# Kernel tuning notes

Hardware: AMD Instinct MI355X
Metric: run time of the kernel (lower is better)

## Reference

```python
import jax, jax.numpy as jnp
import numpy as np

B, CIN, COUT, H, W, K = 16, 16, 16, 256, 256, 3


def setup_inputs() -> dict:
    key = jax.random.key(0)
    k1, k2, k3 = jax.random.split(key, 3)
    x = jax.random.normal(k1, (B, CIN, H, W), dtype=jnp.float32)
    # complex weights stored as two real tensors (out, in, k, k)
    w_real = jax.random.normal(k2, (COUT, CIN, K, K), dtype=jnp.float32)
    w_imag = jax.random.normal(k3, (COUT, CIN, K, K), dtype=jnp.float32)
    return {"x": x, "w_real": w_real, "w_imag": w_imag}


def reference(x, w_real, w_imag):
    # x: (B, Cin, H, W) real; weights: (Cout, Cin, K, K) complex (as two reals)
    Cout, Cin, k, _ = w_real.shape
    h, w = x.shape[-2], x.shape[-1]
    wc = (w_real + 1j * w_imag).astype(jnp.complex64)
    # zero-pad kernel to (Cout, Cin, H, W); batch dim in the original is redundant
    kp = jnp.zeros((Cout, Cin, h, w), dtype=jnp.complex64).at[:, :, :k, :k].set(wc)
    kernel_freq = jnp.fft.fft2(kp)  # (Cout, Cin, H, W) complex
    # out_freq = x.unsqueeze(1) * kernel_freq; sum over in_channels -> (B, Cout, H, W)
    out = jnp.einsum('bihw,oihw->bohw', x.astype(jnp.complex64), kernel_freq)
    # return complex result as stacked (real, imag): shape (2, B, Cout, H, W)
    return jnp.stack([out.real, out.imag])
```

## Files before the change

### kernel.cpp

```cpp
#include <hip/hip_runtime.h>


constexpr int Hd   = 256;
constexpr int Wd   = 256;
constexpr int Bn   = 16;
constexpr int CIN  = 16;
constexpr int COUT = 16;
constexpr int TW   = 32;
constexpr int NTHREADS = 512;

__global__ __launch_bounds__(NTHREADS)
void freq_conv_kernel(const float* __restrict__ x,
                      const float* __restrict__ wr_g,
                      const float* __restrict__ wi_g,
                      float* __restrict__ out)
{
    __shared__ float xs[Bn * CIN * TW];

    const int tid = threadIdx.x;
    const int bid = blockIdx.x;
    const int h  = bid >> 3;
    const int w0 = (bid & 7) * TW;

    float4 stage[4];
#pragma unroll
    for (int t = 0; t < 4; ++t) {
        int lin = t * NTHREADS + tid;
        int row = lin >> 3;
        int seg = lin & 7;
        stage[t] = *reinterpret_cast<const float4*>(
            &x[(size_t)(row * Hd + h) * Wd + w0 + seg * 4]);
    }

    const int o = tid >> 5;
    const int p = tid & 31;
    const int w = w0 + p;

    const float TWO_PI_OVER_N = 6.28318530717958647692f / 256.0f;
    float sh1, ch1, sw1, cw1;
    __sincosf(TWO_PI_OVER_N * (float)h, &sh1, &ch1);
    __sincosf(TWO_PI_OVER_N * (float)w, &sw1, &cw1);
    const float ch[3] = {1.f, ch1, ch1 * ch1 - sh1 * sh1};
    const float sh[3] = {0.f, sh1, 2.f * sh1 * ch1};
    const float cw[3] = {1.f, cw1, cw1 * cw1 - sw1 * sw1};
    const float sw[3] = {0.f, sw1, 2.f * sw1 * cw1};

    float cph[9], sph[9];
#pragma unroll
    for (int pp = 0; pp < 3; ++pp)
#pragma unroll
        for (int qq = 0; qq < 3; ++qq) {
            cph[pp * 3 + qq] = ch[pp] * cw[qq] - sh[pp] * sw[qq];
            sph[pp * 3 + qq] = sh[pp] * cw[qq] + ch[pp] * sw[qq];
        }

    float Kr[CIN], Ki[CIN];
#pragma unroll
    for (int i = 0; i < CIN; ++i) {
        float kr = 0.f, ki = 0.f;
        const float* wr = &wr_g[(o * CIN + i) * 9];
        const float* wi = &wi_g[(o * CIN + i) * 9];
#pragma unroll
        for (int t = 0; t < 9; ++t) {
            const float a = wr[t], bb = wi[t];
            kr += a * cph[t] + bb * sph[t];
            ki += bb * cph[t] - a * sph[t];
        }
        Kr[i] = kr; Ki[i] = ki;
    }

#pragma unroll
    for (int t = 0; t < 4; ++t) {
        int lin = t * NTHREADS + tid;
        reinterpret_cast<float4*>(xs)[lin] = stage[t];
    }
    __syncthreads();

    const size_t hw = (size_t)h * Wd + w;
#pragma unroll
    for (int b = 0; b < Bn; ++b) {
        float ar = 0.f, ai = 0.f;
#pragma unroll
        for (int i = 0; i < CIN; ++i) {
            const float xv = xs[(b * CIN + i) * TW + p];
            ar += xv * Kr[i];
            ai += xv * Ki[i];
        }
        out[((size_t)(b * COUT + o)) * (Hd * Wd) + hw]        = ar;
        out[((size_t)((Bn + b) * COUT + o)) * (Hd * Wd) + hw] = ai;
    }
}

extern "C" void kernel_launch(void* const* d_in, const int* in_sizes, int n_in,
                              void* d_out, int out_size, void* d_ws, size_t ws_size,
                              hipStream_t stream) {
    const float* x  = (const float*)d_in[0];
    const float* wr = (const float*)d_in[1];
    const float* wi = (const float*)d_in[2];
    float* out = (float*)d_out;

    dim3 grid(Hd * (Wd / TW));
    dim3 block(NTHREADS);
    freq_conv_kernel<<<grid, block, 0, stream>>>(x, wr, wi, out);
}
```

Baseline: 208.6 us.

## Use fp16 MFMA for channel contraction with separable precomputed twiddle table

Adds a small prekernel that builds a per-column partial kernel spectrum G (the W-direction DFT of the weights), so the main kernel only combines three row twiddles. The per-pixel Cin contraction is done with 16x16x16 fp16 MFMA instructions instead of scalar FMAs. Outputs are staged through LDS to make the stores coalesced float4 writes. Inputs and kernel values are converted to fp16, which lowers accuracy. It also adds a second launch and an extra workspace read.

```diff
diff --git a/kernel.cpp b/kernel.cpp
--- a/kernel.cpp
+++ b/kernel.cpp
@@ -1,93 +1,126 @@
 #include <hip/hip_runtime.h>
 
 
-constexpr int Hd   = 256;
-constexpr int Wd   = 256;
-constexpr int Bn   = 16;
-constexpr int CIN  = 16;
-constexpr int COUT = 16;
-constexpr int TW   = 32;
-constexpr int NTHREADS = 512;
+typedef _Float16 half4 __attribute__((ext_vector_type(4)));
+typedef float floatx4 __attribute__((ext_vector_type(4)));
 
-__global__ __launch_bounds__(NTHREADS)
-void freq_conv_kernel(const float* __restrict__ x,
-                      const float* __restrict__ wr_g,
-                      const float* __restrict__ wi_g,
-                      float* __restrict__ out)
-{
-    __shared__ float xs[Bn * CIN * TW];
+constexpr int Hd = 256, Wd = 256;
+constexpr int TW = 16;
+constexpr float TWO_PI = 6.283185307179586f;
 
-    const int tid = threadIdx.x;
-    const int bid = blockIdx.x;
-    const int h  = bid >> 3;
-    const int w0 = (bid & 7) * TW;
+__global__ __launch_bounds__(256)
+void build_G(const float* __restrict__ wr, const float* __restrict__ wi,
+             float* __restrict__ G) {
+    const int w = blockIdx.x;
+    const int t = threadIdx.x;
+    const int o = t >> 4, i = t & 15;
+    float s1, c1;
+    __sincosf((TWO_PI / 256.f) * (float)w, &s1, &c1);
+    const float ewr[3] = {1.f, c1, c1 * c1 - s1 * s1};
+    const float ewi[3] = {0.f, -s1, -2.f * s1 * c1};
+    const float* a = &wr[(o * 16 + i) * 9];
+    const float* b = &wi[(o * 16 + i) * 9];
+#pragma unroll
+    for (int p = 0; p < 3; ++p) {
+        float gr = 0.f, gi = 0.f;
+#pragma unroll
+        for (int q = 0; q < 3; ++q) {
+            const float A = a[p * 3 + q], B = b[p * 3 + q];
+            gr += A * ewr[q] - B * ewi[q];
+            gi += A * ewi[q] + B * ewr[q];
+        }
+        reinterpret_cast<float2*>(G)[(w * 3 + p) * 256 + o * 16 + i] =
+            make_float2(gr, gi);
+    }
+}
 
-    float4 stage[4];
+__global__ __launch_bounds__(512)
+void freq_conv_mfma(const float* __restrict__ x, const float* __restrict__ G,
+                    float* __restrict__ out) {
+    __shared__ float XS[TW * 256];
+    __shared__ float CB[2 * 256 * 20];
+
+    const int tid  = threadIdx.x;
+    const int bid  = blockIdx.x;
+    const int h    = bid >> 4;
+    const int w0   = (bid & 15) * TW;
+    const int lane = tid & 63;
+    const int wave = tid >> 6;
+    const int nlo  = lane & 15;
+    const int hi   = lane >> 4;
+
 #pragma unroll
-    for (int t = 0; t < 4; ++t) {
-        int lin = t * NTHREADS + tid;
-        int row = lin >> 3;
-        int seg = lin & 7;
-        stage[t] = *reinterpret_cast<const float4*>(
-            &x[(size_t)(row * Hd + h) * Wd + w0 + seg * 4]);
+    for (int k = 0; k < 2; ++k) {
+        const int idx = k * 512 + tid;
+        const int r   = idx >> 2;
+        const int c   = idx & 3;
+        const float4 v = *reinterpret_cast<const float4*>(
+            &x[(size_t)r * (Hd * Wd) + h * Wd + w0 + 4 * c]);
+        const int rr = (r + 4 * c) & 255;
+        XS[(4 * c + 0) * 256 + rr] = v.x;
+        XS[(4 * c + 1) * 256 + rr] = v.y;
+        XS[(4 * c + 2) * 256 + rr] = v.z;
+        XS[(4 * c + 3) * 256 + rr] = v.w;
     }
 
-    const int o = tid >> 5;
-    const int p = tid & 31;
-    const int w = w0 + p;
+    float s1, c1;
+    __sincosf((TWO_PI / 256.f) * (float)h, &s1, &c1);
+    const float ehr[3] = {1.f, c1, c1 * c1 - s1 * s1};
+    const float ehi[3] = {0.f, -s1, -2.f * s1 * c1};
 
-    const float TWO_PI_OVER_N = 6.28318530717958647692f / 256.0f;
-    float sh1, ch1, sw1, cw1;
-    __sincosf(TWO_PI_OVER_N * (float)h, &sh1, &ch1);
-    __sincosf(TWO_PI_OVER_N * (float)w, &sw1, &cw1);
-    const float ch[3] = {1.f, ch1, ch1 * ch1 - sh1 * sh1};
-    const float sh[3] = {0.f, sh1, 2.f * sh1 * ch1};
-    const float cw[3] = {1.f, cw1, cw1 * cw1 - sw1 * sw1};
-    const float sw[3] = {0.f, sw1, 2.f * sw1 * cw1};
-
-    float cph[9], sph[9];
-#pragma unroll
-    for (int pp = 0; pp < 3; ++pp)
-#pragma unroll
-        for (int qq = 0; qq < 3; ++qq) {
-            cph[pp * 3 + qq] = ch[pp] * cw[qq] - sh[pp] * sw[qq];
-            sph[pp * 3 + qq] = sh[pp] * cw[qq] + ch[pp] * sw[qq];
-        }
-
-    float Kr[CIN], Ki[CIN];
-#pragma unroll
-    for (int i = 0; i < CIN; ++i) {
-        float kr = 0.f, ki = 0.f;
-        const float* wr = &wr_g[(o * CIN + i) * 9];
-        const float* wi = &wi_g[(o * CIN + i) * 9];
-#pragma unroll
-        for (int t = 0; t < 9; ++t) {
-            const float a = wr[t], bb = wi[t];
-            kr += a * cph[t] + bb * sph[t];
-            ki += bb * cph[t] - a * sph[t];
-        }
-        Kr[i] = kr; Ki[i] = ki;
-    }
+    __syncthreads();
 
 #pragma unroll
-    for (int t = 0; t < 4; ++t) {
-        int lin = t * NTHREADS + tid;
-        reinterpret_cast<float4*>(xs)[lin] = stage[t];
+    for (int kk = 0; kk < 2; ++kk) {
+        const int wl = kk * 8 + wave;
+        const int w  = w0 + wl;
+
+        const float4 xa = *reinterpret_cast<const float4*>(
+            &XS[wl * 256 + (((nlo * 16 + 4 * hi) + 4 * (wl >> 2)) & 255)]);
+        const half4 Af = {(_Float16)xa.x, (_Float16)xa.y,
+                          (_Float16)xa.z, (_Float16)xa.w};
+
+        float Kr[4] = {0.f, 0.f, 0.f, 0.f}, Ki[4] = {0.f, 0.f, 0.f, 0.f};
+#pragma unroll
+        for (int p = 0; p < 3; ++p) {
+            const float* gp = &G[((w * 3 + p) * 256 + nlo * 16 + 4 * hi) * 2];
+            const float4 g0 = *reinterpret_cast<const float4*>(gp);
+            const float4 g1 = *reinterpret_cast<const float4*>(gp + 4);
+            const float er = ehr[p], ei = ehi[p];
+            Kr[0] += er * g0.x - ei * g0.y;  Ki[0] += er * g0.y + ei * g0.x;
+            Kr[1] += er * g0.z - ei * g0.w;  Ki[1] += er * g0.w + ei * g0.z;
+            Kr[2] += er * g1.x - ei * g1.y;  Ki[2] += er * g1.y + ei * g1.x;
+            Kr[3] += er * g1.z - ei * g1.w;  Ki[3] += er * g1.w + ei * g1.z;
+        }
+        const half4 Br = {(_Float16)Kr[0], (_Float16)Kr[1],
+                          (_Float16)Kr[2], (_Float16)Kr[3]};
+        const half4 Bi = {(_Float16)Ki[0], (_Float16)Ki[1],
+                          (_Float16)Ki[2], (_Float16)Ki[3]};
+
+        const floatx4 zero = {0.f, 0.f, 0.f, 0.f};
+        const floatx4 Cr = __builtin_amdgcn_mfma_f32_16x16x16f16(Af, Br, zero, 0, 0, 0);
+        const floatx4 Ci = __builtin_amdgcn_mfma_f32_16x16x16f16(Af, Bi, zero, 0, 0, 0);
+
+        const int wsz = (wl + 4 * hi) & 15;
+#pragma unroll
+        for (int r = 0; r < 4; ++r) {
+            const int row = (4 * hi + r) * 16 + nlo;
+            CB[row * 20 + wsz]             = Cr[r];
+            CB[256 * 20 + row * 20 + wsz]  = Ci[r];
+        }
     }
     __syncthreads();
 
-    const size_t hw = (size_t)h * Wd + w;
 #pragma unroll
-    for (int b = 0; b < Bn; ++b) {
-        float ar = 0.f, ai = 0.f;
-#pragma unroll
-        for (int i = 0; i < CIN; ++i) {
-            const float xv = xs[(b * CIN + i) * TW + p];
-            ar += xv * Kr[i];
-            ai += xv * Ki[i];
-        }
-        out[((size_t)(b * COUT + o)) * (Hd * Wd) + hw]        = ar;
-        out[((size_t)((Bn + b) * COUT + o)) * (Hd * Wd) + hw] = ai;
+    for (int pass = 0; pass < 4; ++pass) {
+        const int R  = pass * 128 + (tid >> 2);
+        const int wp = tid & 3;
+        const int b  = (R >> 4) & 15;
+        const int wl_l = (4 * wp + 4 * (b >> 2)) & 15;
+        const float4 v = *reinterpret_cast<const float4*>(
+            &CB[(R >> 8) * (256 * 20) + (R & 255) * 20 + wl_l]);
+        *reinterpret_cast<float4*>(
+            &out[(size_t)R * (Hd * Wd) + h * Wd + w0 + 4 * wp]) = v;
     }
 }
 
@@ -98,8 +131,8 @@
     const float* wr = (const float*)d_in[1];
     const float* wi = (const float*)d_in[2];
     float* out = (float*)d_out;
+    float* G   = (float*)d_ws;
 
-    dim3 grid(Hd * (Wd / TW));
-    dim3 block(NTHREADS);
-    freq_conv_kernel<<<grid, block, 0, stream>>>(x, wr, wi, out);
+    build_G<<<256, 256, 0, stream>>>(wr, wi, G);
+    freq_conv_mfma<<<Hd * (Wd / TW), 512, 0, stream>>>(x, G, out);
 }
```

Measured after the change: 231.5 us. 1.11x slower.
